# Kernel tuning notes

Hardware: AMD Instinct MI355X
Metric: run time of the kernel (lower is better)

The kernel has to match this reference:

```python
import jax, jax.numpy as jnp
import numpy as np

B, S_RAW, S_SUM, D_IN, H, NH = 32, 1024, 128, 300, 256, 4
DH = (2 * H) // NH  # per-head dim = 128


def _lstm_dir(x, Wih, Whh, b, reverse):
    """Single-direction LSTM (PyTorch gate order i,f,g,o). x: [B,S,D] -> [B,S,H]."""
    xg = jnp.einsum('bsd,gd->bsg', x, Wih) + b          # precompute input gates [B,S,4H]
    xg = jnp.swapaxes(xg, 0, 1)                          # [S,B,4H]
    Hh = Whh.shape[1]
    bsz = x.shape[0]

    def step(carry, g):
        h, c = carry
        gates = g + h @ Whh.T
        i, f, gg, o = jnp.split(gates, 4, axis=-1)
        c = jax.nn.sigmoid(f) * c + jax.nn.sigmoid(i) * jnp.tanh(gg)
        h = jax.nn.sigmoid(o) * jnp.tanh(c)
        return (h, c), h

    init = (jnp.zeros((bsz, Hh), x.dtype), jnp.zeros((bsz, Hh), x.dtype))
    _, hs = jax.lax.scan(step, init, xg, reverse=reverse)  # hs aligned with input time order
    return jnp.swapaxes(hs, 0, 1)


def _bilstm(x, pf, pb):
    return jnp.concatenate([_lstm_dir(x, *pf, False), _lstm_dir(x, *pb, True)], axis=-1)


def setup_inputs() -> dict:
    key = jax.random.key(0)
    ks = jax.random.split(key, 24)
    s_lstm = 1.0 / np.sqrt(H)
    s_proj = 1.0 / np.sqrt(2 * H)
    d = {}
    d['in_raw'] = jax.random.normal(ks[0], (B, S_RAW, D_IN), jnp.float32)
    d['in_sum'] = jax.random.normal(ks[1], (B, S_SUM, D_IN), jnp.float32)
    d['len_raw'] = jax.random.randint(ks[2], (B,), 0, S_RAW)
    d['len_sum'] = jax.random.randint(ks[3], (B,), 0, S_SUM)
    i = 4
    for name in ['raw_f', 'raw_b', 'sum_f', 'sum_b']:
        d[name + '_Wih'] = jax.random.uniform(ks[i], (4 * H, D_IN), jnp.float32, -s_lstm, s_lstm); i += 1
        d[name + '_Whh'] = jax.random.uniform(ks[i], (4 * H, H), jnp.float32, -s_lstm, s_lstm); i += 1
        d[name + '_b'] = jax.random.uniform(ks[i], (4 * H,), jnp.float32, -s_lstm, s_lstm); i += 1
    d['Wq'] = jax.random.uniform(ks[i], (NH, 2 * H, DH), jnp.float32, -s_proj, s_proj); i += 1
    d['Wk'] = jax.random.uniform(ks[i], (NH, 2 * H, DH), jnp.float32, -s_proj, s_proj); i += 1
    d['Wv'] = jax.random.uniform(ks[i], (NH, 2 * H, DH), jnp.float32, -s_proj, s_proj)
    return d


def reference(in_raw, in_sum, len_raw, len_sum,
              raw_f_Wih, raw_f_Whh, raw_f_b, raw_b_Wih, raw_b_Whh, raw_b_b,
              sum_f_Wih, sum_f_Whh, sum_f_b, sum_b_Wih, sum_b_Whh, sum_b_b,
              Wq, Wk, Wv):
    # BiLSTM encoders (dropout is identity in eval mode)
    out_raw = _bilstm(in_raw, (raw_f_Wih, raw_f_Whh, raw_f_b), (raw_b_Wih, raw_b_Whh, raw_b_b))  # [B,Sr,2H]
    out_sum = _bilstm(in_sum, (sum_f_Wih, sum_f_Whh, sum_f_b), (sum_b_Wih, sum_b_Whh, sum_b_b))  # [B,Ss,2H]

    # mean_pooling over the first len_sum[i] timesteps (lengths clamped to >=1)
    lens = jnp.maximum(len_sum, 1)
    mask = (jnp.arange(S_SUM)[None, :] < lens[:, None]).astype(out_sum.dtype)  # [B,Ss]
    sum_vec = jnp.einsum('bsd,bs->bd', out_sum, mask) / lens.astype(out_sum.dtype)[:, None]  # [B,2H]

    # per-head cross-attention against the single pooled summary vector (rank-1 attention)
    q = jnp.einsum('bsd,hde->hbse', out_raw, Wq)   # [NH,B,Sr,DH]
    k = jnp.einsum('bd,hde->hbe', sum_vec, Wk)     # [NH,B,DH]
    v = jnp.einsum('bd,hde->hbe', sum_vec, Wv)     # [NH,B,DH]
    scores = jnp.einsum('hbse,hbe->hbs', q, k)     # [NH,B,Sr] (use_divide_dk=False)
    attn = jax.nn.softmax(scores, axis=-1)
    rst = attn[..., None] * v[:, :, None, :] + q   # outer product + residual, [NH,B,Sr,DH]

    # concat heads along last dim -> [B,Sr,2H]
    rst = jnp.transpose(rst, (1, 2, 0, 3)).reshape(B, S_RAW, NH * DH)
    return rst
```

## Files before the change

### kernel.cpp

```cpp
#include <hip/hip_runtime.h>

typedef _Float16 f16;
typedef _Float16 half2t __attribute__((ext_vector_type(2)));
typedef _Float16 half8 __attribute__((ext_vector_type(8)));
typedef float f32x4 __attribute__((ext_vector_type(4)));

#define KP 320
#define DIN 300
#define SRAW 1024
#define SSUM 128

static constexpr size_t OFF_XG_RAW  = 0;
static constexpr size_t OFF_XG_SUM  = OFF_XG_RAW + (size_t)2*32*1024*1024*2;
static constexpr size_t OFF_OUT_RAW = OFF_XG_SUM + (size_t)2*32*128*1024*2;
static constexpr size_t OFF_OUT_SUM = OFF_OUT_RAW + (size_t)32*1024*512*2;
static constexpr size_t OFF_A_RAW   = OFF_OUT_SUM + (size_t)32*128*512*2;
static constexpr size_t OFF_A_SUM   = OFF_A_RAW + (size_t)32768*KP*2;
static constexpr size_t OFF_BIH_RAW = OFF_A_SUM + (size_t)4096*KP*2;
static constexpr size_t OFF_BIH_SUM = OFF_BIH_RAW + (size_t)2048*KP*2;
static constexpr size_t OFF_WHH     = OFF_BIH_SUM + (size_t)2048*KP*2;
static constexpr size_t OFF_WQ      = OFF_WHH + (size_t)4*32*1024*8*2;
static constexpr size_t OFF_KB      = OFF_WQ + (size_t)512*512*2;
static constexpr size_t OFF_VB      = OFF_KB + (size_t)4*32*128*4;
static constexpr size_t OFF_ATTN    = OFF_VB + (size_t)4*32*128*4;
static constexpr size_t WS_NEED     = OFF_ATTN + (size_t)4*32*1024*4;

__global__ void pack_kernel(
    const float* __restrict__ in_raw, const float* __restrict__ in_sum,
    const float* __restrict__ wih_rf, const float* __restrict__ wih_rb,
    const float* __restrict__ wih_sf, const float* __restrict__ wih_sb,
    const float* __restrict__ whh_rf, const float* __restrict__ whh_rb,
    const float* __restrict__ whh_sf, const float* __restrict__ whh_sb,
    const float* __restrict__ wq,
    f16* __restrict__ a_raw, f16* __restrict__ a_sum,
    f16* __restrict__ bih_raw, f16* __restrict__ bih_sum,
    f16* __restrict__ whh16, f16* __restrict__ wq16)
{
  constexpr size_t N1 = (size_t)32768*KP;
  constexpr size_t N2 = (size_t)4096*KP;
  constexpr size_t N3 = (size_t)2048*KP;
  constexpr size_t N5 = (size_t)4*32*1024*8;
  constexpr size_t N6 = (size_t)512*512;
  const size_t TOT = N1+N2+N3+N3+N5+N6;
  const size_t stride = (size_t)gridDim.x*blockDim.x;
  for (size_t i = (size_t)blockIdx.x*blockDim.x + threadIdx.x; i < TOT; i += stride) {
    size_t j = i;
    if (j < N1) {
      size_t m = j/KP, k = j - m*KP;
      a_raw[j] = (f16)(k < DIN ? in_raw[m*DIN + k] : 0.f);
      continue;
    }
    j -= N1;
    if (j < N2) {
      size_t m = j/KP, k = j - m*KP;
      a_sum[j] = (f16)(k < DIN ? in_sum[m*DIN + k] : 0.f);
      continue;
    }
    j -= N2;
    if (j < N3) {
      size_t n = j/KP, k = j - n*KP;
      float v = 0.f;
      if (k < DIN) v = (n < 1024) ? wih_rf[n*DIN + k] : wih_rb[(n-1024)*DIN + k];
      bih_raw[j] = (f16)v;
      continue;
    }
    j -= N3;
    if (j < N3) {
      size_t n = j/KP, k = j - n*KP;
      float v = 0.f;
      if (k < DIN) v = (n < 1024) ? wih_sf[n*DIN + k] : wih_sb[(n-1024)*DIN + k];
      bih_sum[j] = (f16)v;
      continue;
    }
    j -= N3;
    if (j < N5) {
      int ed  = (int)(j >> 18);
      int q   = (int)((j >> 13) & 31);
      int row = (int)((j >> 3) & 1023);
      int ii  = (int)(j & 7);
      const float* src = (ed==0)?whh_rf:(ed==1)?whh_rb:(ed==2)?whh_sf:whh_sb;
      whh16[j] = (f16)src[(size_t)row*256 + q*8 + ii];
      continue;
    }
    j -= N5;
    {
      int n = (int)(j >> 9), k = (int)(j & 511);
      int h = n >> 7, dh = n & 127;
      wq16[j] = (f16)wq[((size_t)h*512 + k)*128 + dh];
    }
  }
}

template<int EPI>
__global__ __launch_bounds__(256) void gemm_kernel(
    const f16* __restrict__ A, const f16* __restrict__ Bm,
    float* __restrict__ Cf, f16* __restrict__ Cx,
    const float* __restrict__ bias0, const float* __restrict__ bias1,
    int K, int ldcN, size_t dirStride)
{
  __shared__ __align__(16) f16 As[128*40];
  __shared__ __align__(16) f16 Bs[128*40];
  const int tid = threadIdx.x;
  const int m0 = blockIdx.x*128, n0 = blockIdx.y*128;
  const int w = tid >> 6, lane = tid & 63;
  const int wm = w >> 1, wn = w & 1;
  const int lr = lane & 15, lk = lane >> 4;
  f32x4 acc[4][4] = {};
  const int nsteps = K >> 5;
  for (int kt = 0; kt < nsteps; ++kt) {
    __syncthreads();
    #pragma unroll
    for (int it = 0; it < 2; ++it) {
      int c = tid + it*256;
      int r = c >> 2, kc = c & 3;
      *(uint4*)&As[r*40 + kc*8] = *(const uint4*)&A[(size_t)(m0+r)*K + kt*32 + kc*8];
      *(uint4*)&Bs[r*40 + kc*8] = *(const uint4*)&Bm[(size_t)(n0+r)*K + kt*32 + kc*8];
    }
    __syncthreads();
    half8 af[4], bf[4];
    #pragma unroll
    for (int mt = 0; mt < 4; ++mt) af[mt] = *(const half8*)&As[(wm*64 + mt*16 + lr)*40 + lk*8];
    #pragma unroll
    for (int nt = 0; nt < 4; ++nt) bf[nt] = *(const half8*)&Bs[(wn*64 + nt*16 + lr)*40 + lk*8];
    #pragma unroll
    for (int mt = 0; mt < 4; ++mt)
      #pragma unroll
      for (int nt = 0; nt < 4; ++nt)
        acc[mt][nt] = __builtin_amdgcn_mfma_f32_16x16x32_f16(af[mt], bf[nt], acc[mt][nt], 0, 0, 0);
  }
  const int rb = lk*4;
  #pragma unroll
  for (int mt = 0; mt < 4; ++mt) {
    #pragma unroll
    for (int nt = 0; nt < 4; ++nt) {
      int n = n0 + wn*64 + nt*16 + lr;
      int mloc = m0 + wm*64 + mt*16 + rb;
      if (EPI == 0) {
        #pragma unroll
        for (int r = 0; r < 4; ++r)
          Cf[(size_t)(mloc+r)*ldcN + n] = acc[mt][nt][r];
      } else {
        int dir = n >> 10, cc = n & 1023;
        float bs = (dir ? bias1 : bias0)[cc];
        f16* dst = Cx + (size_t)dir*dirStride;
        #pragma unroll
        for (int r = 0; r < 4; ++r)
          dst[(size_t)(mloc+r)*1024 + cc] = (f16)(acc[mt][nt][r] + bs);
      }
    }
  }
}

#define NREG 24
#define NLDS 5
#define NGLB 3

__device__ __forceinline__ float dot8(float acc, uint4 wv, uint4 hv) {
#if __has_builtin(__builtin_amdgcn_fdot2)
  union { uint4 u; half2t h[4]; } W, Hh;
  W.u = wv; Hh.u = hv;
  #pragma unroll
  for (int i = 0; i < 4; ++i) acc = __builtin_amdgcn_fdot2(W.h[i], Hh.h[i], acc, false);
#else
  union { uint4 u; f16 h[8]; } W, Hh;
  W.u = wv; Hh.u = hv;
  #pragma unroll
  for (int i = 0; i < 8; ++i) acc += (float)W.h[i]*(float)Hh.h[i];
#endif
  return acc;
}

__device__ __forceinline__ float sigmoid_f(float x) {
  float e = __expf(-x);
  return __builtin_amdgcn_rcpf(1.f + e);
}
__device__ __forceinline__ float tanh_f(float x) {
  float e = __expf(2.f * x);
  return 1.f - 2.f * __builtin_amdgcn_rcpf(e + 1.f);
}

__device__ __forceinline__ void pin4(uint4& v) {
  asm volatile("" : "+v"(v.x), "+v"(v.y), "+v"(v.z), "+v"(v.w));
}

__global__ __launch_bounds__(512, 2) void lstm_kernel(
    const f16* __restrict__ whh16,
    const f16* __restrict__ xg_raw, const f16* __restrict__ xg_sum,
    f16* __restrict__ out_raw, f16* __restrict__ out_sum)
{
  const int wg = blockIdx.x;
  const int e = wg >> 6, r2 = wg & 63, d = r2 >> 5, b = r2 & 31;
  const int S = e ? SSUM : SRAW;
  const int t = threadIdx.x;
  const f16* wbase = whh16 + (size_t)(e*2+d)*(32*1024*8);
  const uint4* wreg_g = (const uint4*)wbase;
  const uint4* wlds_g = (const uint4*)(wbase + (size_t)NREG*1024*8);
  const uint4* wglb_g = (const uint4*)(wbase + (size_t)(NREG+NLDS)*1024*8);
  const f16* xg = (e ? xg_sum : xg_raw) + ((size_t)(d*32 + b))*(size_t)S*1024;
  f16* outp = (e ? out_sum : out_raw) + (size_t)b*S*512 + d*256;

  __shared__ __align__(16) f16 wl[NLDS*1024*8];
  __shared__ __align__(16) f16 hl[256];
  __shared__ float exf[256];
  __shared__ float exo[256];

  uint4 wrA[NREG], wrB[NREG];
  #pragma unroll
  for (int j = 0; j < NREG; ++j) {
    wrA[j] = wreg_g[j*1024 + t];
    wrB[j] = wreg_g[j*1024 + t + 512];
  }
  #pragma unroll
  for (int j = 0; j < NREG; ++j) { pin4(wrA[j]); pin4(wrB[j]); }
  for (int i = t; i < NLDS*1024; i += 512) ((uint4*)wl)[i] = wlds_g[i];
  if (t < 256) hl[t] = (f16)0.f;
  float cst = 0.f;
  const int s0 = d ? (S - 1) : 0;
  f16 xcA = xg[(size_t)s0*1024 + t];
  f16 xcB = xg[(size_t)s0*1024 + t + 512];
  __syncthreads();

  for (int st = 0; st < S; ++st) {
    const int s = d ? (S - 1 - st) : st;
    uint4 gA0 = wglb_g[t],        gB0 = wglb_g[t + 512];
    uint4 gA1 = wglb_g[1024 + t], gB1 = wglb_g[1024 + t + 512];
    uint4 gA2 = wglb_g[2048 + t], gB2 = wglb_g[2048 + t + 512];
    f16 xnA = (f16)0.f, xnB = (f16)0.f;
    if (st + 1 < S) {
      const int sn = d ? (S - 2 - st) : (st + 1);
      xnA = xg[(size_t)sn*1024 + t];
      xnB = xg[(size_t)sn*1024 + t + 512];
    }
    float accA = (float)xcA, accB = (float)xcB;
    #pragma unroll
    for (int q = 0; q < NREG; ++q) {
      uint4 hv = *(const uint4*)&hl[q*8];
      accA = dot8(accA, wrA[q], hv);
      accB = dot8(accB, wrB[q], hv);
    }
    #pragma unroll
    for (int j = 0; j < NLDS; ++j) {
      uint4 hv = *(const uint4*)&hl[(NREG + j)*8];
      uint4 wvA = *(const uint4*)&wl[((size_t)(j*1024 + t))*8];
      uint4 wvB = *(const uint4*)&wl[((size_t)(j*1024 + t + 512))*8];
      accA = dot8(accA, wvA, hv);
      accB = dot8(accB, wvB, hv);
    }
    { uint4 hv = *(const uint4*)&hl[(NREG+NLDS+0)*8]; accA = dot8(accA, gA0, hv); accB = dot8(accB, gB0, hv); }
    { uint4 hv = *(const uint4*)&hl[(NREG+NLDS+1)*8]; accA = dot8(accA, gA1, hv); accB = dot8(accB, gB1, hv); }
    { uint4 hv = *(const uint4*)&hl[(NREG+NLDS+2)*8]; accA = dot8(accA, gA2, hv); accB = dot8(accB, gB2, hv); }
    float aA = sigmoid_f(accA);
    float aB;
    if (t < 256) {
      aB = tanh_f(accB);
    } else {
      aB = sigmoid_f(accB);
      exf[t - 256] = aA;
      exo[t - 256] = aB;
    }
    xcA = xnA; xcB = xnB;
    __syncthreads();
    if (t < 256) {
      cst = exf[t]*cst + aA*aB;
      float hval = exo[t]*tanh_f(cst);
      f16 hf = (f16)hval;
      hl[t] = hf;
      outp[(size_t)s*512 + t] = hf;
    }
    __syncthreads();
  }
}

__global__ __launch_bounds__(256) void pool_kv_kernel(
    const f16* __restrict__ out_sum, const int* __restrict__ len_sum,
    const float* __restrict__ Wk, const float* __restrict__ Wv,
    float* __restrict__ kb, float* __restrict__ vb)
{
  const int b = blockIdx.x, t = threadIdx.x;
  __shared__ float sv[512];
  int len = len_sum[b]; if (len < 1) len = 1;
  float a0 = 0.f, a1 = 0.f;
  for (int s = 0; s < len; ++s) {
    const f16* row = out_sum + ((size_t)b*SSUM + s)*512;
    a0 += (float)row[t];
    a1 += (float)row[t+256];
  }
  float inv = 1.f/(float)len;
  sv[t] = a0*inv; sv[t+256] = a1*inv;
  __syncthreads();
  #pragma unroll
  for (int half = 0; half < 2; ++half) {
    int o = t + half*256;
    int h = o >> 7, dh = o & 127;
    const float* wkp = Wk + (size_t)h*512*128 + dh;
    const float* wvp = Wv + (size_t)h*512*128 + dh;
    float ak = 0.f, av = 0.f;
    for (int e2 = 0; e2 < 512; ++e2) {
      float sve = sv[e2];
      ak += sve*wkp[(size_t)e2*128];
      av += sve*wvp[(size_t)e2*128];
    }
    kb[((size_t)h*32 + b)*128 + dh] = ak;
    vb[((size_t)h*32 + b)*128 + dh] = av;
  }
}

__global__ __launch_bounds__(256) void attn_kernel(
    const float* __restrict__ q, const float* __restrict__ kb, float* __restrict__ attn)
{
  const int hb = blockIdx.x;
  const int h = hb >> 5, b = hb & 31;
  const int t = threadIdx.x;
  __shared__ __align__(16) float kk[128];
  __shared__ float red[4];
  if (t < 128) kk[t] = kb[(size_t)hb*128 + t];
  __syncthreads();
  float vals[4];
  #pragma unroll
  for (int i = 0; i < 4; ++i) {
    int s = t + i*256;
    const float4* qp = (const float4*)(q + ((size_t)b*1024 + s)*512 + h*128);
    const float4* kp = (const float4*)kk;
    float a = 0.f;
    #pragma unroll
    for (int e2 = 0; e2 < 32; ++e2) {
      float4 qq = qp[e2], kx = kp[e2];
      a += qq.x*kx.x + qq.y*kx.y + qq.z*kx.z + qq.w*kx.w;
    }
    vals[i] = a;
  }
  float m = fmaxf(fmaxf(vals[0], vals[1]), fmaxf(vals[2], vals[3]));
  for (int o = 1; o < 64; o <<= 1) m = fmaxf(m, __shfl_xor(m, o));
  if ((t & 63) == 0) red[t >> 6] = m;
  __syncthreads();
  m = fmaxf(fmaxf(red[0], red[1]), fmaxf(red[2], red[3]));
  __syncthreads();
  float ex[4], lsum = 0.f;
  #pragma unroll
  for (int i = 0; i < 4; ++i) { ex[i] = __expf(vals[i] - m); lsum += ex[i]; }
  for (int o = 1; o < 64; o <<= 1) lsum += __shfl_xor(lsum, o);
  if ((t & 63) == 0) red[t >> 6] = lsum;
  __syncthreads();
  float inv = 1.f/(red[0] + red[1] + red[2] + red[3]);
  #pragma unroll
  for (int i = 0; i < 4; ++i) attn[(size_t)hb*1024 + t + i*256] = ex[i]*inv;
}

__global__ __launch_bounds__(256) void final_kernel(
    float* __restrict__ out, const float* __restrict__ attn, const float* __restrict__ vb)
{
  const size_t TOT4 = (size_t)32*1024*512/4;
  const size_t stride = (size_t)gridDim.x*blockDim.x;
  for (size_t i = (size_t)blockIdx.x*blockDim.x + threadIdx.x; i < TOT4; i += stride) {
    int c4 = (int)(i & 127);
    int h = c4 >> 5;
    size_t srow = i >> 7;
    int b = (int)(srow >> 10), s = (int)(srow & 1023);
    float a = attn[((size_t)h*32 + b)*1024 + s];
    float4 vv = ((const float4*)vb)[((size_t)h*32 + b)*32 + (c4 & 31)];
    float4 qq = ((float4*)out)[i];
    qq.x += a*vv.x; qq.y += a*vv.y; qq.z += a*vv.z; qq.w += a*vv.w;
    ((float4*)out)[i] = qq;
  }
}

extern "C" void kernel_launch(void* const* d_in, const int* in_sizes, int n_in,
                              void* d_out, int out_size, void* d_ws, size_t ws_size,
                              hipStream_t stream)
{
  const float* in_raw = (const float*)d_in[0];
  const float* in_sum = (const float*)d_in[1];
  const int*  len_sum = (const int*)d_in[3];
  const float* rf_wih = (const float*)d_in[4];
  const float* rf_whh = (const float*)d_in[5];
  const float* rf_b   = (const float*)d_in[6];
  const float* rb_wih = (const float*)d_in[7];
  const float* rb_whh = (const float*)d_in[8];
  const float* rb_b   = (const float*)d_in[9];
  const float* sf_wih = (const float*)d_in[10];
  const float* sf_whh = (const float*)d_in[11];
  const float* sf_b   = (const float*)d_in[12];
  const float* sb_wih = (const float*)d_in[13];
  const float* sb_whh = (const float*)d_in[14];
  const float* sb_b   = (const float*)d_in[15];
  const float* wq     = (const float*)d_in[16];
  const float* wk     = (const float*)d_in[17];
  const float* wv     = (const float*)d_in[18];

  if (ws_size < WS_NEED) return;

  char* ws = (char*)d_ws;
  f16* xg_raw_p  = (f16*)(ws + OFF_XG_RAW);
  f16* xg_sum_p  = (f16*)(ws + OFF_XG_SUM);
  f16* out_raw_p = (f16*)(ws + OFF_OUT_RAW);
  f16* out_sum_p = (f16*)(ws + OFF_OUT_SUM);
  f16* a_raw_p   = (f16*)(ws + OFF_A_RAW);
  f16* a_sum_p   = (f16*)(ws + OFF_A_SUM);
  f16* bih_raw_p = (f16*)(ws + OFF_BIH_RAW);
  f16* bih_sum_p = (f16*)(ws + OFF_BIH_SUM);
  f16* whh16_p   = (f16*)(ws + OFF_WHH);
  f16* wq16_p    = (f16*)(ws + OFF_WQ);
  float* kb_p    = (float*)(ws + OFF_KB);
  float* vb_p    = (float*)(ws + OFF_VB);
  float* attn_p  = (float*)(ws + OFF_ATTN);
  float* qout    = (float*)d_out;

  pack_kernel<<<4096, 256, 0, stream>>>(
      in_raw, in_sum, rf_wih, rb_wih, sf_wih, sb_wih,
      rf_whh, rb_whh, sf_whh, sb_whh, wq,
      a_raw_p, a_sum_p, bih_raw_p, bih_sum_p, whh16_p, wq16_p);

  gemm_kernel<1><<<dim3(256, 16), 256, 0, stream>>>(
      a_raw_p, bih_raw_p, nullptr, xg_raw_p, rf_b, rb_b, KP, 0, (size_t)32*1024*1024);
  gemm_kernel<1><<<dim3(32, 16), 256, 0, stream>>>(
      a_sum_p, bih_sum_p, nullptr, xg_sum_p, sf_b, sb_b, KP, 0, (size_t)32*128*1024);

  lstm_kernel<<<128, 512, 0, stream>>>(whh16_p, xg_raw_p, xg_sum_p, out_raw_p, out_sum_p);

  gemm_kernel<0><<<dim3(256, 4), 256, 0, stream>>>(
      out_raw_p, wq16_p, qout, nullptr, nullptr, nullptr, 512, 512, 0);

  pool_kv_kernel<<<32, 256, 0, stream>>>(out_sum_p, len_sum, wk, wv, kb_p, vb_p);
  attn_kernel<<<128, 256, 0, stream>>>(qout, kb_p, attn_p);
  final_kernel<<<4096, 256, 0, stream>>>(qout, attn_p, vb_p);
}
```

Measured before the change: 2.077 ms.

## Split LSTM recurrent matvec across 8-lane K-slices with DPP reductions

Restructures the recurrent LSTM step so each group of 8 lanes splits the K dimension of the hidden-state dot product, with partial sums combined by DPP cross-lane adds. The Whh weights are repacked into a matching row-group/K-slice layout. The input-gate GEMM epilogue is changed to interleave the four gates per unit so one thread loads all four with a single 8-byte read. The hidden state is replicated in LDS with padding to reduce bank conflicts. Each lane now holds a K slice of several rows rather than full rows, and the per-row weight split between registers, LDS and global memory changes, which alters register pressure and the number of reductions and selects per step.

New measurement: 2.335 ms. +12.4%, slower.

```diff
diff --git a/kernel.cpp b/kernel.cpp
--- a/kernel.cpp
+++ b/kernel.cpp
@@ -19,7 +19,7 @@
 static constexpr size_t OFF_BIH_RAW = OFF_A_SUM + (size_t)4096*KP*2;
 static constexpr size_t OFF_BIH_SUM = OFF_BIH_RAW + (size_t)2048*KP*2;
 static constexpr size_t OFF_WHH     = OFF_BIH_SUM + (size_t)2048*KP*2;
-static constexpr size_t OFF_WQ      = OFF_WHH + (size_t)4*32*1024*8*2;
+static constexpr size_t OFF_WQ      = OFF_WHH + (size_t)4*64*512*8*2;
 static constexpr size_t OFF_KB      = OFF_WQ + (size_t)512*512*2;
 static constexpr size_t OFF_VB      = OFF_KB + (size_t)4*32*128*4;
 static constexpr size_t OFF_ATTN    = OFF_VB + (size_t)4*32*128*4;
@@ -39,7 +39,7 @@
   constexpr size_t N1 = (size_t)32768*KP;
   constexpr size_t N2 = (size_t)4096*KP;
   constexpr size_t N3 = (size_t)2048*KP;
-  constexpr size_t N5 = (size_t)4*32*1024*8;
+  constexpr size_t N5 = (size_t)4*64*512*8;
   constexpr size_t N6 = (size_t)512*512;
   const size_t TOT = N1+N2+N3+N3+N5+N6;
   const size_t stride = (size_t)gridDim.x*blockDim.x;
@@ -74,12 +74,16 @@
     }
     j -= N3;
     if (j < N5) {
-      int ed  = (int)(j >> 18);
-      int q   = (int)((j >> 13) & 31);
-      int row = (int)((j >> 3) & 1023);
-      int ii  = (int)(j & 7);
+      int ed = (int)(j >> 18);
+      int c  = (int)((j >> 12) & 63);
+      int t  = (int)((j >> 3) & 511);
+      int ii = (int)(j & 7);
+      int jrow = c >> 2, q = c & 3;
+      int rg = t >> 3, ks = t & 7;
+      int row = rg*16 + jrow;
+      int col = ks*32 + q*8 + ii;
       const float* src = (ed==0)?whh_rf:(ed==1)?whh_rb:(ed==2)?whh_sf:whh_sb;
-      whh16[j] = (f16)src[(size_t)row*256 + q*8 + ii];
+      whh16[j] = (f16)src[(size_t)row*256 + col];
       continue;
     }
     j -= N5;
@@ -141,19 +145,19 @@
           Cf[(size_t)(mloc+r)*ldcN + n] = acc[mt][nt][r];
       } else {
         int dir = n >> 10, cc = n & 1023;
+        int gate = cc >> 8, u = cc & 255;
         float bs = (dir ? bias1 : bias0)[cc];
         f16* dst = Cx + (size_t)dir*dirStride;
         #pragma unroll
         for (int r = 0; r < 4; ++r)
-          dst[(size_t)(mloc+r)*1024 + cc] = (f16)(acc[mt][nt][r] + bs);
+          dst[(size_t)(mloc+r)*1024 + u*4 + gate] = (f16)(acc[mt][nt][r] + bs);
       }
     }
   }
 }
 
-#define NREG 24
-#define NLDS 5
-#define NGLB 3
+#define RROWS 10
+#define LROWS 3
 
 __device__ __forceinline__ float dot8(float acc, uint4 wv, uint4 hv) {
 #if __has_builtin(__builtin_amdgcn_fdot2)
@@ -183,7 +187,20 @@
   asm volatile("" : "+v"(v.x), "+v"(v.y), "+v"(v.z), "+v"(v.w));
 }
 
-__global__ __launch_bounds__(512, 2) void lstm_kernel(
+template<int CTRL>
+__device__ __forceinline__ float dpp_add(float v) {
+  int m = __builtin_amdgcn_update_dpp(0, __builtin_bit_cast(int, v), CTRL, 0xf, 0xf, true);
+  return v + __builtin_bit_cast(float, m);
+}
+__device__ __forceinline__ float reduce8(float v) {
+  v = dpp_add<0xB1>(v);
+  v = dpp_add<0x4E>(v);
+  v = dpp_add<0x141>(v);
+  return v;
+}
+
+__global__ void __launch_bounds__(512) __attribute__((amdgpu_waves_per_eu(2, 2)))
+lstm_kernel(
     const f16* __restrict__ whh16,
     const f16* __restrict__ xg_raw, const f16* __restrict__ xg_sum,
     f16* __restrict__ out_raw, f16* __restrict__ out_sum)
@@ -192,79 +209,113 @@
   const int e = wg >> 6, r2 = wg & 63, d = r2 >> 5, b = r2 & 31;
   const int S = e ? SSUM : SRAW;
   const int t = threadIdx.x;
-  const f16* wbase = whh16 + (size_t)(e*2+d)*(32*1024*8);
-  const uint4* wreg_g = (const uint4*)wbase;
-  const uint4* wlds_g = (const uint4*)(wbase + (size_t)NREG*1024*8);
-  const uint4* wglb_g = (const uint4*)(wbase + (size_t)(NREG+NLDS)*1024*8);
+  const int rg = t >> 3, ks = t & 7;
+  const uint4* wb = (const uint4*)(whh16 + (size_t)(e*2+d)*(64*512*8));
   const f16* xg = (e ? xg_sum : xg_raw) + ((size_t)(d*32 + b))*(size_t)S*1024;
   f16* outp = (e ? out_sum : out_raw) + (size_t)b*S*512 + d*256;
 
-  __shared__ __align__(16) f16 wl[NLDS*1024*8];
-  __shared__ __align__(16) f16 hl[256];
-  __shared__ float exf[256];
-  __shared__ float exo[256];
-
-  uint4 wrA[NREG], wrB[NREG];
-  #pragma unroll
-  for (int j = 0; j < NREG; ++j) {
-    wrA[j] = wreg_g[j*1024 + t];
-    wrB[j] = wreg_g[j*1024 + t + 512];
-  }
-  #pragma unroll
-  for (int j = 0; j < NREG; ++j) { pin4(wrA[j]); pin4(wrB[j]); }
-  for (int i = t; i < NLDS*1024; i += 512) ((uint4*)wl)[i] = wlds_g[i];
-  if (t < 256) hl[t] = (f16)0.f;
+  __shared__ __align__(16) uint4 wl[LROWS*4*512];
+  __shared__ float pre[1024];
+  __shared__ __align__(16) f16 hrep[4*264];
+
+  #pragma unroll
+  for (int c = 0; c < LROWS*4; ++c) wl[c*512 + t] = wb[(RROWS*4 + c)*512 + t];
+  uint4 wr[RROWS*4];
+  #pragma unroll
+  for (int c = 0; c < RROWS*4; ++c) wr[c] = wb[c*512 + t];
+  #pragma unroll
+  for (int c = 0; c < RROWS*4; ++c) pin4(wr[c]);
+
+  if (t < 256) {
+    #pragma unroll
+    for (int cpy = 0; cpy < 4; ++cpy) hrep[cpy*264 + t] = (f16)0.f;
+  }
   float cst = 0.f;
-  const int s0 = d ? (S - 1) : 0;
-  f16 xcA = xg[(size_t)s0*1024 + t];
-  f16 xcB = xg[(size_t)s0*1024 + t + 512];
+  const int hbyte = (ks >> 1)*528 + ks*64;
+  const int preS = ((rg >> 4) << 8) + ((rg & 15) << 4);
   __syncthreads();
 
   for (int st = 0; st < S; ++st) {
     const int s = d ? (S - 1 - st) : st;
-    uint4 gA0 = wglb_g[t],        gB0 = wglb_g[t + 512];
-    uint4 gA1 = wglb_g[1024 + t], gB1 = wglb_g[1024 + t + 512];
-    uint4 gA2 = wglb_g[2048 + t], gB2 = wglb_g[2048 + t + 512];
-    f16 xnA = (f16)0.f, xnB = (f16)0.f;
-    if (st + 1 < S) {
-      const int sn = d ? (S - 2 - st) : (st + 1);
-      xnA = xg[(size_t)sn*1024 + t];
-      xnB = xg[(size_t)sn*1024 + t + 512];
-    }
-    float accA = (float)xcA, accB = (float)xcB;
-    #pragma unroll
-    for (int q = 0; q < NREG; ++q) {
-      uint4 hv = *(const uint4*)&hl[q*8];
-      accA = dot8(accA, wrA[q], hv);
-      accB = dot8(accB, wrB[q], hv);
-    }
-    #pragma unroll
-    for (int j = 0; j < NLDS; ++j) {
-      uint4 hv = *(const uint4*)&hl[(NREG + j)*8];
-      uint4 wvA = *(const uint4*)&wl[((size_t)(j*1024 + t))*8];
-      uint4 wvB = *(const uint4*)&wl[((size_t)(j*1024 + t + 512))*8];
-      accA = dot8(accA, wvA, hv);
-      accB = dot8(accB, wvB, hv);
-    }
-    { uint4 hv = *(const uint4*)&hl[(NREG+NLDS+0)*8]; accA = dot8(accA, gA0, hv); accB = dot8(accB, gB0, hv); }
-    { uint4 hv = *(const uint4*)&hl[(NREG+NLDS+1)*8]; accA = dot8(accA, gA1, hv); accB = dot8(accB, gB1, hv); }
-    { uint4 hv = *(const uint4*)&hl[(NREG+NLDS+2)*8]; accA = dot8(accA, gA2, hv); accB = dot8(accB, gB2, hv); }
-    float aA = sigmoid_f(accA);
-    float aB;
+    asm volatile("" ::: "memory");
+
+    uint2 xq;
+    if (t < 256) xq = *(const uint2*)(xg + ((size_t)s*1024 + t*4));
+
+    uint4 gA[4], gB[4], gC[4];
+    #pragma unroll
+    for (int q = 0; q < 4; ++q) gA[q] = wb[(52 + q)*512 + t];
+    #pragma unroll
+    for (int q = 0; q < 4; ++q) gB[q] = wb[(56 + q)*512 + t];
+
+    uint4 hv[4];
+    #pragma unroll
+    for (int q = 0; q < 4; ++q)
+      hv[q] = *(const uint4*)((const char*)hrep + hbyte + q*16);
+
+    float pa = 0.f, pb = 0.f;
+
+    #pragma unroll
+    for (int j = 0; j < RROWS; ++j) {
+      float rs = 0.f;
+      #pragma unroll
+      for (int q = 0; q < 4; ++q) rs = dot8(rs, wr[j*4 + q], hv[q]);
+      rs = reduce8(rs);
+      if (j < 8) { pa = (ks == j) ? rs : pa; }
+      else       { pb = (ks == j - 8) ? rs : pb; }
+    }
+    #pragma unroll
+    for (int q = 0; q < 4; ++q) gC[q] = wb[(60 + q)*512 + t];
+    #pragma unroll
+    for (int j = RROWS; j < RROWS + LROWS; ++j) {
+      float rs = 0.f;
+      #pragma unroll
+      for (int q = 0; q < 4; ++q) rs = dot8(rs, wl[((j - RROWS)*4 + q)*512 + t], hv[q]);
+      rs = reduce8(rs);
+      pb = (ks == j - 8) ? rs : pb;
+    }
+    {
+      float rs = 0.f;
+      #pragma unroll
+      for (int q = 0; q < 4; ++q) rs = dot8(rs, gA[q], hv[q]);
+      rs = reduce8(rs);
+      pb = (ks == 5) ? rs : pb;
+    }
+    {
+      float rs = 0.f;
+      #pragma unroll
+      for (int q = 0; q < 4; ++q) rs = dot8(rs, gB[q], hv[q]);
+      rs = reduce8(rs);
+      pb = (ks == 6) ? rs : pb;
+    }
+    {
+      float rs = 0.f;
+      #pragma unroll
+      for (int q = 0; q < 4; ++q) rs = dot8(rs, gC[q], hv[q]);
+      rs = reduce8(rs);
+      pb = (ks == 7) ? rs : pb;
+    }
+
+    pre[preS + ks]     = pa;
+    pre[preS + 8 + ks] = pb;
+    __syncthreads();
+
     if (t < 256) {
-      aB = tanh_f(accB);
-    } else {
-      aB = sigmoid_f(accB);
-      exf[t - 256] = aA;
-      exo[t - 256] = aB;
-    }
-    xcA = xnA; xcB = xnB;
-    __syncthreads();
-    if (t < 256) {
-      cst = exf[t]*cst + aA*aB;
-      float hval = exo[t]*tanh_f(cst);
+      half2t x01 = __builtin_bit_cast(half2t, xq.x);
+      half2t x23 = __builtin_bit_cast(half2t, xq.y);
+      float vi = pre[t]       + (float)x01[0];
+      float vf = pre[256 + t] + (float)x01[1];
+      float vg = pre[512 + t] + (float)x23[0];
+      float vo = pre[768 + t] + (float)x23[1];
+      float ig = sigmoid_f(vi);
+      float fg = sigmoid_f(vf);
+      float gg = tanh_f(vg);
+      float og = sigmoid_f(vo);
+      cst = fg*cst + ig*gg;
+      float hval = og*tanh_f(cst);
       f16 hf = (f16)hval;
-      hl[t] = hf;
+      #pragma unroll
+      for (int cpy = 0; cpy < 4; ++cpy) hrep[cpy*264 + t] = hf;
       outp[(size_t)s*512 + t] = hf;
     }
     __syncthreads();
```
